# Kernel optimization log

Measured on AMD Instinct MI355X. Metric: run time of the kernel, lower is better.

Reference implementation:

```python
import jax, jax.numpy as jnp
import numpy as np

B, S, D, H = 2, 2048, 1024, 16
DK = D // H  # 64


def setup_inputs() -> dict:
    key = jax.random.key(0)
    ks = jax.random.split(key, 4)
    scale = 1.0 / np.sqrt(D)
    return {
        "q_input": jax.random.normal(ks[0], (B, S, D), dtype=jnp.float32),
        "W_q": jax.random.normal(ks[1], (D, D), dtype=jnp.float32) * scale,
        "b_q": jnp.zeros((D,), dtype=jnp.float32),
        "W_k": jax.random.normal(ks[2], (D, D), dtype=jnp.float32) * scale,
        "b_k": jnp.zeros((D,), dtype=jnp.float32),
        "W_v": jax.random.normal(ks[3], (D, D), dtype=jnp.float32) * scale,
        "b_v": jnp.zeros((D,), dtype=jnp.float32),
    }


def reference(q_input, W_q, b_q, W_k, b_k, W_v, b_v):
    # Self-attention: k_input and v_input default to q_input in the torch module.
    # nn.Linear computes x @ W.T + b
    q = q_input @ W_q.T + b_q
    k = q_input @ W_k.T + b_k
    v = q_input @ W_v.T + b_v

    # [B,S,D] -> [B,H,S,DK]
    def split_heads(x):
        return x.reshape(B, S, H, DK).transpose(0, 2, 1, 3)

    qh, kh, vh = split_heads(q), split_heads(k), split_heads(v)

    # scores [B,H,S,S]; causal mask added BEFORE scaling (as in source; -inf invariant)
    scores = jnp.einsum("bhqd,bhkd->bhqk", qh, kh)
    causal = jnp.tril(jnp.ones((S, S), dtype=bool))
    scores = jnp.where(causal[None, None], scores, -jnp.inf)
    scores = scores / jnp.sqrt(jnp.float32(DK))
    probs = jax.nn.softmax(scores, axis=-1)
    z = jnp.einsum("bhqk,bhkd->bhqd", probs, vh)  # [B,H,S,DK]
    # [B,H,S,DK] -> [B,S,H,DK] -> [B,S,D]
    return z.transpose(0, 2, 1, 3).reshape(B, S, D)
```

## Files before the change

### kernel.cpp

```cpp
#include <hip/hip_runtime.h>
#include <hip/hip_bf16.h>
#include <stdint.h>

typedef __attribute__((ext_vector_type(8))) short short8;
typedef __attribute__((ext_vector_type(4))) short short4v;
typedef __attribute__((ext_vector_type(4))) float f32x4;

#define B_ 2
#define S_ 2048
#define D_ 1024
#define H_ 16
#define DK_ 64
#define M_ (B_*S_)

#define WS_QKV   0
#define WS_XB    12582912
#define WS_WB    16777216

#define QSCALE (0.125f * 1.44269504088896f)

#define GLL16(g, l) __builtin_amdgcn_global_load_lds( \
    (const __attribute__((address_space(1))) void*)(g), \
    (__attribute__((address_space(3))) void*)(l), 16, 0, 0)

#define WAIT_VM0 asm volatile("s_waitcnt vmcnt(0)" ::: "memory")
#define WAIT_VM4 asm volatile("s_waitcnt vmcnt(4)" ::: "memory")
#define WAIT_VM8 asm volatile("s_waitcnt vmcnt(8)" ::: "memory")
#define WAIT_LGKM0 asm volatile("s_waitcnt lgkmcnt(0)" ::: "memory")
#define BARRIER_RAW asm volatile("s_barrier" ::: "memory")

static __device__ __forceinline__ short f2bf(float f){
  union { float f; unsigned u; } x; x.f = f;
  unsigned r = x.u + 0x7fff + ((x.u >> 16) & 1);
  return (short)(r >> 16);
}

__global__ __launch_bounds__(256) void cvt_bf16(
    const float* __restrict__ X,  const float* __restrict__ Wq,
    const float* __restrict__ Wk, const float* __restrict__ Wv,
    short* __restrict__ ws)
{
  const int z = blockIdx.z;
  const float* src; short* dst; int n;
  if (z == 0)      { src = X;  dst = ws + WS_XB;               n = M_*D_; }
  else if (z == 1) { src = Wq; dst = ws + WS_WB;               n = D_*D_; }
  else if (z == 2) { src = Wk; dst = ws + WS_WB + D_*D_;       n = D_*D_; }
  else             { src = Wv; dst = ws + WS_WB + 2*(D_*D_);   n = D_*D_; }
  const int stride = gridDim.x * blockDim.x * 4;
  for (int i = (blockIdx.x * blockDim.x + threadIdx.x) * 4; i < n; i += stride) {
    float4 v = *(const float4*)(src + i);
    short4v o;
    o.x = f2bf(v.x); o.y = f2bf(v.y); o.z = f2bf(v.z); o.w = f2bf(v.w);
    *(short4v*)(dst + i) = o;
  }
}

__global__ __launch_bounds__(512, 2) void qkv_gemm(
    const short* __restrict__ ws_in,
    const float* __restrict__ bq, const float* __restrict__ bk,
    const float* __restrict__ bv, short* __restrict__ qkv)
{
  const int z = blockIdx.z;
  const short* X  = ws_in + WS_XB;
  const short* Wm = ws_in + WS_WB + (size_t)z * (D_*D_);
  short* out = qkv + (size_t)z * (M_*D_);

  __shared__ __align__(16) short lds[65536];

  const int t = threadIdx.x;
  const int w = t >> 6, lane = t & 63;
  const int quad = lane >> 4, l16 = lane & 15;
  const int wm = w >> 2, wn = w & 3;
  const int m0 = blockIdx.y * 256, n0 = blockIdx.x * 256;

  const int rl = t >> 2;
  const int sl = (t & 3) ^ (rl & 3);
  const short* sA0 = X  + (size_t)(m0 + rl) * D_ + sl*8;
  const short* sA1 = sA0 + (size_t)128 * D_;
  const short* sB0 = Wm + (size_t)(n0 + rl) * D_ + sl*8;
  const short* sB1 = sB0 + (size_t)128 * D_;
  const int ldsw = w << 9;

  const int swz = quad ^ (l16 & 3);

  f32x4 acc[8][4];
  #pragma unroll
  for (int i=0;i<8;i++)
    #pragma unroll
    for (int j=0;j<4;j++) acc[i][j] = (f32x4){0.f,0.f,0.f,0.f};

  #pragma unroll
  for (int p=0;p<3;p++){
    GLL16(sA0 + p*32, lds + p*16384 + ldsw);
    GLL16(sA1 + p*32, lds + p*16384 + 4096 + ldsw);
    GLL16(sB0 + p*32, lds + p*16384 + 8192 + ldsw);
    GLL16(sB1 + p*32, lds + p*16384 + 12288 + ldsw);
  }
  WAIT_VM8;
  BARRIER_RAW;

  for (int kt = 0; kt < 32; kt++) {
    const int bf = kt & 3;
    const short* bufA = lds + bf*16384;
    const short* bufB = bufA + 8192;
    const int tb = (kt + 3) & 3;
    const int ko2 = (kt + 3) * 32;
    const bool st = (kt + 3) < 32;

    short8 aF[4], bF[4];
    #pragma unroll
    for (int mf=0; mf<4; mf++)
      aF[mf] = *(const short8*)(bufA + (wm*128 + mf*16 + l16)*32 + swz*8);
    #pragma unroll
    for (int nf=0; nf<4; nf++)
      bF[nf] = *(const short8*)(bufB + (wn*64 + nf*16 + l16)*32 + swz*8);
    if (st) {
      GLL16(sA0 + ko2, lds + tb*16384 + ldsw);
      GLL16(sA1 + ko2, lds + tb*16384 + 4096 + ldsw);
    }
    BARRIER_RAW;
    WAIT_LGKM0;
    __builtin_amdgcn_s_setprio(1);
    #pragma unroll
    for (int mf=0; mf<4; mf++)
      #pragma unroll
      for (int nf=0; nf<4; nf++)
        acc[mf][nf] = __builtin_amdgcn_mfma_f32_16x16x32_bf16(aF[mf], bF[nf], acc[mf][nf], 0,0,0);
    __builtin_amdgcn_s_setprio(0);
    BARRIER_RAW;

    #pragma unroll
    for (int mf=0; mf<4; mf++)
      aF[mf] = *(const short8*)(bufA + (wm*128 + 64 + mf*16 + l16)*32 + swz*8);
    if (st) {
      GLL16(sB0 + ko2, lds + tb*16384 + 8192 + ldsw);
      GLL16(sB1 + ko2, lds + tb*16384 + 12288 + ldsw);
    }
    BARRIER_RAW;
    WAIT_LGKM0;
    __builtin_amdgcn_s_setprio(1);
    #pragma unroll
    for (int mf=0; mf<4; mf++)
      #pragma unroll
      for (int nf=0; nf<4; nf++)
        acc[4+mf][nf] = __builtin_amdgcn_mfma_f32_16x16x32_bf16(aF[mf], bF[nf], acc[4+mf][nf], 0,0,0);
    __builtin_amdgcn_s_setprio(0);
    if      (kt < 29)  { WAIT_VM8; }
    else if (kt == 29) { WAIT_VM4; }
    else if (kt == 30) { WAIT_VM0; }
    BARRIER_RAW;
  }

  __syncthreads();

  if (z != 2) {
    const float scale = (z==0) ? QSCALE : 1.0f;
    const float* bias = (z==0) ? bq : bk;
    float bv4[4];
    #pragma unroll
    for (int nf=0; nf<4; nf++) bv4[nf] = bias[n0 + wn*64 + nf*16 + l16];
    short* ep = lds;
    #pragma unroll
    for (int p=0; p<2; p++){
      if (wm == p){
        #pragma unroll
        for (int mf=0; mf<8; mf++)
          #pragma unroll
          for (int nf=0; nf<4; nf++)
            #pragma unroll
            for (int i=0; i<4; i++)
              ep[(mf*16 + quad*4 + i)*264 + wn*64 + nf*16 + l16] =
                  f2bf((acc[mf][nf][i] + bv4[nf]) * scale);
      }
      __syncthreads();
      #pragma unroll
      for (int it=0; it<8; it++){
        const int cid = it*512 + t;
        const int row = cid >> 5, cc = cid & 31;
        short8 vv = *(const short8*)(ep + row*264 + cc*8);
        const int m = m0 + p*128 + row, bidx = m >> 11, s = m & 2047;
        const int n = n0 + cc*8, h = n >> 6, dd = n & 63;
        *(short8*)(out + (((size_t)(bidx*H_ + h))*S_ + s)*DK_ + dd) = vv;
      }
      __syncthreads();
    }
  } else {
    float bv4[4];
    #pragma unroll
    for (int nf=0; nf<4; nf++) bv4[nf] = bv[n0 + wn*64 + nf*16 + l16];
    short* ep = lds;
    #pragma unroll
    for (int p=0; p<2; p++){
      if (wm == p){
        #pragma unroll
        for (int mf=0; mf<8; mf++)
          #pragma unroll
          for (int nf=0; nf<4; nf++)
            #pragma unroll
            for (int i=0; i<4; i++)
              ep[(wn*64 + nf*16 + l16)*136 + mf*16 + quad*4 + i] =
                  f2bf(acc[mf][nf][i] + bv4[nf]);
      }
      __syncthreads();
      #pragma unroll
      for (int it=0; it<8; it++){
        const int cid = it*512 + t;
        const int row = cid >> 4, cc = cid & 15;
        short8 vv = *(const short8*)(ep + row*136 + cc*8);
        const int n = n0 + row, h = n >> 6, dd = n & 63;
        const int m0p = m0 + p*128;
        const int bidx = m0p >> 11;
        const int s = (m0p & 2047) + cc*8;
        *(short8*)(out + (((size_t)(bidx*H_ + h))*DK_ + dd)*S_ + s) = vv;
      }
      __syncthreads();
    }
  }
}

__global__ __launch_bounds__(256, 3) void attn(
    const short* __restrict__ qkv, float* __restrict__ out)
{
  const int bh = blockIdx.y;
  const int qt = (gridDim.x - 1) - blockIdx.x;
  const short* Q  = qkv + (size_t)bh * (S_*DK_);
  const short* K  = Q + (size_t)(M_*D_);
  const short* VT = qkv + (size_t)(2*M_*D_) + (size_t)bh * (DK_*S_);

  __shared__ short Kbuf[2][4096];
  __shared__ short Vbuf[2][4096];
  __shared__ short Ps[8192];

  const int t = threadIdx.x;
  const int w = t >> 6, lane = t & 63;
  const int quad = lane >> 4, l16 = lane & 15;
  const int sw = l16 & 7;
  const int lr = lane >> 3, lc = lane & 7;
  const int csrc = lc ^ lr;

  short8 bq[2][2];
  #pragma unroll
  for (int kc=0;kc<2;kc++)
    #pragma unroll
    for (int mt=0;mt<2;mt++)
      bq[kc][mt] = *(const short8*)(Q + (size_t)(qt*128 + w*32 + mt*16 + l16)*DK_
                                      + (kc*4 + quad)*8);

  const int nkt = 2*qt + 2;
  #pragma unroll
  for (int j=0;j<2;j++){
    const int rb = (j*4 + w)*8;
    GLL16(K  + (size_t)(rb + lr)*DK_ + csrc*8, &Kbuf[0][0] + rb*64);
    GLL16(VT + (size_t)(rb + lr)*S_  + csrc*8, &Vbuf[0][0] + rb*64);
  }

  f32x4 o[2][4];
  float lsum[2];
  #pragma unroll
  for (int mt=0;mt<2;mt++){
    #pragma unroll
    for (int nd=0;nd<4;nd++) o[mt][nd] = (f32x4){0.f,0.f,0.f,0.f};
    lsum[mt] = 0.f;
  }

  const int pw_half = (quad & 1) * 4;
  const int pw_ckb  = quad >> 1;
  int cur = 0;

  for (int kt = 0; kt < nkt; kt++){
    WAIT_VM0;
    BARRIER_RAW;
    const int nxt = cur ^ 1;
    if (kt + 1 < nkt) {
      const int kb2 = (kt+1)*64;
      short* Kn = &Kbuf[nxt][0];
      short* Vn = &Vbuf[nxt][0];
      #pragma unroll
      for (int j=0;j<2;j++){
        const int rb = (j*4 + w)*8;
        GLL16(K  + (size_t)(kb2 + rb + lr)*DK_ + csrc*8, Kn + rb*64);
        GLL16(VT + (size_t)(rb + lr)*S_ + kb2 + csrc*8,  Vn + rb*64);
      }
    }
    const short* Kc = &Kbuf[cur][0];
    const short* Vc = &Vbuf[cur][0];
    const int kb = kt*64;

    f32x4 sc[4][2];
    #pragma unroll
    for (int ntk=0;ntk<4;ntk++)
      #pragma unroll
      for (int mt=0;mt<2;mt++) sc[ntk][mt] = (f32x4){0.f,0.f,0.f,0.f};
    #pragma unroll
    for (int kc=0;kc<2;kc++){
      const int xch = (kc*4 + quad) ^ sw;
      short8 ak[4];
      #pragma unroll
      for (int ntk=0;ntk<4;ntk++)
        ak[ntk] = *(const short8*)(Kc + (ntk*16 + l16)*64 + xch*8);
      #pragma unroll
      for (int ntk=0;ntk<4;ntk++)
        #pragma unroll
        for (int mt=0;mt<2;mt++)
          sc[ntk][mt] = __builtin_amdgcn_mfma_f32_16x16x32_bf16(ak[ntk], bq[kc][mt], sc[ntk][mt], 0,0,0);
    }

    const int q0w = qt*128 + w*32;
    if (kb + 63 > q0w) {
      #pragma unroll
      for (int ntk=0;ntk<4;ntk++)
        #pragma unroll
        for (int mt=0;mt<2;mt++){
          const int qg = q0w + mt*16 + l16;
          #pragma unroll
          for (int i=0;i<4;i++){
            const int kg = kb + ntk*16 + quad*4 + i;
            if (kg > qg) sc[ntk][mt][i] = -3.0e38f;
          }
        }
    }

    #pragma unroll
    for (int mt=0;mt<2;mt++){
      const int r = w*32 + mt*16 + l16;
      #pragma unroll
      for (int ntk=0;ntk<4;ntk++){
        float p0 = __builtin_amdgcn_exp2f(sc[ntk][mt][0]);
        float p1 = __builtin_amdgcn_exp2f(sc[ntk][mt][1]);
        float p2 = __builtin_amdgcn_exp2f(sc[ntk][mt][2]);
        float p3 = __builtin_amdgcn_exp2f(sc[ntk][mt][3]);
        lsum[mt] += (p0+p1) + (p2+p3);
        unsigned lo = __builtin_amdgcn_perm(__float_as_uint(p1), __float_as_uint(p0), 0x07060302u);
        unsigned hi = __builtin_amdgcn_perm(__float_as_uint(p3), __float_as_uint(p2), 0x07060302u);
        const int slot = (ntk*2 + pw_ckb) ^ sw;
        *(uint2*)(Ps + r*64 + slot*8 + pw_half) = make_uint2(lo, hi);
      }
    }
    asm volatile("" ::: "memory");

    #pragma unroll
    for (int kc=0;kc<2;kc++){
      const int xch = (kc*4 + quad) ^ sw;
      short8 pa[2], vb[4];
      #pragma unroll
      for (int mt=0;mt<2;mt++)
        pa[mt] = *(const short8*)(Ps + (w*32 + mt*16 + l16)*64 + xch*8);
      #pragma unroll
      for (int nd=0;nd<4;nd++)
        vb[nd] = *(const short8*)(Vc + (nd*16 + l16)*64 + xch*8);
      #pragma unroll
      for (int mt=0;mt<2;mt++)
        #pragma unroll
        for (int nd=0;nd<4;nd++)
          o[mt][nd] = __builtin_amdgcn_mfma_f32_16x16x32_bf16(pa[mt], vb[nd], o[mt][nd], 0,0,0);
    }
    cur = nxt;
  }

  const int bb = bh >> 4, h = bh & 15;
  float linv[2];
  #pragma unroll
  for (int mt=0;mt<2;mt++){
    float rs = lsum[mt];
    rs += __shfl_xor(rs, 16, 64);
    rs += __shfl_xor(rs, 32, 64);
    linv[mt] = 1.0f / rs;
  }
  #pragma unroll
  for (int mt=0;mt<2;mt++){
    #pragma unroll
    for (int i=0;i<4;i++){
      const float lw = __shfl(linv[mt], (quad<<4) + (quad<<2) + i, 64);
      const int q = qt*128 + w*32 + mt*16 + quad*4 + i;
      #pragma unroll
      for (int nd=0;nd<4;nd++){
        const int d = nd*16 + l16;
        out[ ((size_t)bb*S_ + q)*D_ + h*DK_ + d ] = o[mt][nd][i] * lw;
      }
    }
  }
}

extern "C" void kernel_launch(void* const* d_in, const int* in_sizes, int n_in,
                              void* d_out, int out_size, void* d_ws, size_t ws_size,
                              hipStream_t stream)
{
  (void)in_sizes; (void)n_in; (void)out_size; (void)ws_size;
  const float* X  = (const float*)d_in[0];
  const float* Wq = (const float*)d_in[1];
  const float* bq = (const float*)d_in[2];
  const float* Wk = (const float*)d_in[3];
  const float* bk = (const float*)d_in[4];
  const float* Wv = (const float*)d_in[5];
  const float* bv = (const float*)d_in[6];
  short* ws  = (short*)d_ws;
  float* out = (float*)d_out;

  dim3 g0(1024, 1, 4);
  cvt_bf16<<<g0, dim3(256,1,1), 0, stream>>>(X, Wq, Wk, Wv, ws);
  dim3 g1(D_/256, M_/256, 3);
  qkv_gemm<<<g1, dim3(512,1,1), 0, stream>>>(ws, bq, bk, bv, ws + WS_QKV);
  dim3 g2(S_/128, B_*H_);
  attn<<<g2, dim3(256,1,1), 0, stream>>>(ws + WS_QKV, out);
}
```

Baseline: 176.4 us.

## Rewrite attention with 32x32 MFMA, register-resident P, and 256-row query tiles

Switches the attention kernel from 16x16x32 to 32x32x16 bf16 MFMA tiles and grows each block to 512 threads covering 256 query rows. The probabilities now go straight from the score accumulators into the PV A-operand through v_cvt_pk_bf16 and v_permlane32_swap, which removes the LDS round-trip and its shared buffer. Warps whose key tile lies wholly above the causal diagonal skip their compute but still take part in the loads and barriers. The cost is fewer blocks, which means less parallelism and coarser causal load balance across the grid, plus more work per warp.

```diff
diff --git a/kernel.cpp b/kernel.cpp
--- a/kernel.cpp
+++ b/kernel.cpp
@@ -5,6 +5,7 @@
 typedef __attribute__((ext_vector_type(8))) short short8;
 typedef __attribute__((ext_vector_type(4))) short short4v;
 typedef __attribute__((ext_vector_type(4))) float f32x4;
+typedef __attribute__((ext_vector_type(16))) float f32x16;
 
 #define B_ 2
 #define S_ 2048
@@ -218,166 +219,126 @@
   }
 }
 
-__global__ __launch_bounds__(256, 3) void attn(
+__global__ __launch_bounds__(512, 2) void attn(
     const short* __restrict__ qkv, float* __restrict__ out)
 {
   const int bh = blockIdx.y;
-  const int qt = (gridDim.x - 1) - blockIdx.x;
+  const int qt = 7 - blockIdx.x;
   const short* Q  = qkv + (size_t)bh * (S_*DK_);
   const short* K  = Q + (size_t)(M_*D_);
   const short* VT = qkv + (size_t)(2*M_*D_) + (size_t)bh * (DK_*S_);
 
   __shared__ short Kbuf[2][4096];
   __shared__ short Vbuf[2][4096];
-  __shared__ short Ps[8192];
 
   const int t = threadIdx.x;
   const int w = t >> 6, lane = t & 63;
-  const int quad = lane >> 4, l16 = lane & 15;
-  const int sw = l16 & 7;
-  const int lr = lane >> 3, lc = lane & 7;
-  const int csrc = lc ^ lr;
-
-  short8 bq[2][2];
+  const int l32 = lane & 31, h = lane >> 5;
+
+  const int q0w = qt*256 + w*32;
+
+  short8 bq[4];
   #pragma unroll
-  for (int kc=0;kc<2;kc++)
-    #pragma unroll
-    for (int mt=0;mt<2;mt++)
-      bq[kc][mt] = *(const short8*)(Q + (size_t)(qt*128 + w*32 + mt*16 + l16)*DK_
-                                      + (kc*4 + quad)*8);
-
-  const int nkt = 2*qt + 2;
-  #pragma unroll
-  for (int j=0;j<2;j++){
-    const int rb = (j*4 + w)*8;
-    GLL16(K  + (size_t)(rb + lr)*DK_ + csrc*8, &Kbuf[0][0] + rb*64);
-    GLL16(VT + (size_t)(rb + lr)*S_  + csrc*8, &Vbuf[0][0] + rb*64);
-  }
-
-  f32x4 o[2][4];
-  float lsum[2];
-  #pragma unroll
-  for (int mt=0;mt<2;mt++){
-    #pragma unroll
-    for (int nd=0;nd<4;nd++) o[mt][nd] = (f32x4){0.f,0.f,0.f,0.f};
-    lsum[mt] = 0.f;
-  }
-
-  const int pw_half = (quad & 1) * 4;
-  const int pw_ckb  = quad >> 1;
-  int cur = 0;
+  for (int dc=0; dc<4; dc++)
+    bq[dc] = *(const short8*)(Q + (size_t)(q0w + l32)*DK_ + dc*16 + h*8);
+
+  const int sr  = w*8 + (lane >> 3);
+  const int sc8 = ((lane & 7) ^ (lane >> 3)) * 8;
+
+  const int nkt = 4*(qt+1);
+  GLL16(K  + (size_t)sr*DK_ + sc8, &Kbuf[0][0] + w*512);
+  GLL16(VT + (size_t)sr*S_  + sc8, &Vbuf[0][0] + w*512);
+
+  f32x16 o0 = {0.f,0.f,0.f,0.f,0.f,0.f,0.f,0.f,0.f,0.f,0.f,0.f,0.f,0.f,0.f,0.f};
+  f32x16 o1 = o0;
+  float lsum = 0.f;
+  const int xrow = l32 & 7;
 
   for (int kt = 0; kt < nkt; kt++){
+    const int cur = kt & 1;
     WAIT_VM0;
     BARRIER_RAW;
-    const int nxt = cur ^ 1;
     if (kt + 1 < nkt) {
       const int kb2 = (kt+1)*64;
-      short* Kn = &Kbuf[nxt][0];
-      short* Vn = &Vbuf[nxt][0];
-      #pragma unroll
-      for (int j=0;j<2;j++){
-        const int rb = (j*4 + w)*8;
-        GLL16(K  + (size_t)(kb2 + rb + lr)*DK_ + csrc*8, Kn + rb*64);
-        GLL16(VT + (size_t)(rb + lr)*S_ + kb2 + csrc*8,  Vn + rb*64);
-      }
-    }
+      GLL16(K  + (size_t)(kb2 + sr)*DK_ + sc8, &Kbuf[cur^1][0] + w*512);
+      GLL16(VT + (size_t)sr*S_ + kb2 + sc8,    &Vbuf[cur^1][0] + w*512);
+    }
+    const int kb = kt*64;
+    if (kb > q0w + 31) continue;
+
     const short* Kc = &Kbuf[cur][0];
     const short* Vc = &Vbuf[cur][0];
-    const int kb = kt*64;
-
-    f32x4 sc[4][2];
-    #pragma unroll
-    for (int ntk=0;ntk<4;ntk++)
-      #pragma unroll
-      for (int mt=0;mt<2;mt++) sc[ntk][mt] = (f32x4){0.f,0.f,0.f,0.f};
-    #pragma unroll
-    for (int kc=0;kc<2;kc++){
-      const int xch = (kc*4 + quad) ^ sw;
-      short8 ak[4];
-      #pragma unroll
-      for (int ntk=0;ntk<4;ntk++)
-        ak[ntk] = *(const short8*)(Kc + (ntk*16 + l16)*64 + xch*8);
-      #pragma unroll
-      for (int ntk=0;ntk<4;ntk++)
-        #pragma unroll
-        for (int mt=0;mt<2;mt++)
-          sc[ntk][mt] = __builtin_amdgcn_mfma_f32_16x16x32_bf16(ak[ntk], bq[kc][mt], sc[ntk][mt], 0,0,0);
-    }
-
-    const int q0w = qt*128 + w*32;
+
+    f32x16 s[2];
+    s[0] = o0 - o0;
+    s[1] = s[0];
+    #pragma unroll
+    for (int dc=0; dc<4; dc++){
+      const int xk = ((dc*2 + h) ^ xrow)*8;
+      short8 a0 = *(const short8*)(Kc + l32*64 + xk);
+      short8 a1 = *(const short8*)(Kc + (32 + l32)*64 + xk);
+      s[0] = __builtin_amdgcn_mfma_f32_32x32x16_bf16(a0, bq[dc], s[0], 0,0,0);
+      s[1] = __builtin_amdgcn_mfma_f32_32x32x16_bf16(a1, bq[dc], s[1], 0,0,0);
+    }
+
     if (kb + 63 > q0w) {
-      #pragma unroll
-      for (int ntk=0;ntk<4;ntk++)
-        #pragma unroll
-        for (int mt=0;mt<2;mt++){
-          const int qg = q0w + mt*16 + l16;
-          #pragma unroll
-          for (int i=0;i<4;i++){
-            const int kg = kb + ntk*16 + quad*4 + i;
-            if (kg > qg) sc[ntk][mt][i] = -3.0e38f;
-          }
-        }
-    }
-
-    #pragma unroll
-    for (int mt=0;mt<2;mt++){
-      const int r = w*32 + mt*16 + l16;
-      #pragma unroll
-      for (int ntk=0;ntk<4;ntk++){
-        float p0 = __builtin_amdgcn_exp2f(sc[ntk][mt][0]);
-        float p1 = __builtin_amdgcn_exp2f(sc[ntk][mt][1]);
-        float p2 = __builtin_amdgcn_exp2f(sc[ntk][mt][2]);
-        float p3 = __builtin_amdgcn_exp2f(sc[ntk][mt][3]);
-        lsum[mt] += (p0+p1) + (p2+p3);
-        unsigned lo = __builtin_amdgcn_perm(__float_as_uint(p1), __float_as_uint(p0), 0x07060302u);
-        unsigned hi = __builtin_amdgcn_perm(__float_as_uint(p3), __float_as_uint(p2), 0x07060302u);
-        const int slot = (ntk*2 + pw_ckb) ^ sw;
-        *(uint2*)(Ps + r*64 + slot*8 + pw_half) = make_uint2(lo, hi);
-      }
-    }
-    asm volatile("" ::: "memory");
-
-    #pragma unroll
-    for (int kc=0;kc<2;kc++){
-      const int xch = (kc*4 + quad) ^ sw;
-      short8 pa[2], vb[4];
-      #pragma unroll
-      for (int mt=0;mt<2;mt++)
-        pa[mt] = *(const short8*)(Ps + (w*32 + mt*16 + l16)*64 + xch*8);
-      #pragma unroll
-      for (int nd=0;nd<4;nd++)
-        vb[nd] = *(const short8*)(Vc + (nd*16 + l16)*64 + xch*8);
-      #pragma unroll
-      for (int mt=0;mt<2;mt++)
-        #pragma unroll
-        for (int nd=0;nd<4;nd++)
-          o[mt][nd] = __builtin_amdgcn_mfma_f32_16x16x32_bf16(pa[mt], vb[nd], o[mt][nd], 0,0,0);
-    }
-    cur = nxt;
-  }
-
-  const int bb = bh >> 4, h = bh & 15;
-  float linv[2];
+      const int qg = q0w + l32;
+      #pragma unroll
+      for (int r=0; r<16; r++){
+        const int k0 = kb + (r&3) + 8*(r>>2) + 4*h;
+        if (k0      > qg) s[0][r] = -3.0e38f;
+        if (k0 + 32 > qg) s[1][r] = -3.0e38f;
+      }
+    }
+
+    short8 pf[4];
+    #pragma unroll
+    for (int mk=0; mk<2; mk++){
+      #pragma unroll
+      for (int u=0; u<2; u++){
+        float p0 = __builtin_amdgcn_exp2f(s[mk][8*u+0]);
+        float p1 = __builtin_amdgcn_exp2f(s[mk][8*u+1]);
+        float p2 = __builtin_amdgcn_exp2f(s[mk][8*u+2]);
+        float p3 = __builtin_amdgcn_exp2f(s[mk][8*u+3]);
+        float p4 = __builtin_amdgcn_exp2f(s[mk][8*u+4]);
+        float p5 = __builtin_amdgcn_exp2f(s[mk][8*u+5]);
+        float p6 = __builtin_amdgcn_exp2f(s[mk][8*u+6]);
+        float p7 = __builtin_amdgcn_exp2f(s[mk][8*u+7]);
+        lsum += ((p0+p1)+(p2+p3)) + ((p4+p5)+(p6+p7));
+        unsigned X0, X1, Y0, Y1;
+        asm("v_cvt_pk_bf16_f32 %0, %1, %2" : "=v"(X0) : "v"(p0), "v"(p1));
+        asm("v_cvt_pk_bf16_f32 %0, %1, %2" : "=v"(X1) : "v"(p2), "v"(p3));
+        asm("v_cvt_pk_bf16_f32 %0, %1, %2" : "=v"(Y0) : "v"(p4), "v"(p5));
+        asm("v_cvt_pk_bf16_f32 %0, %1, %2" : "=v"(Y1) : "v"(p6), "v"(p7));
+        asm("v_permlane32_swap_b32 %0, %1" : "+v"(X0), "+v"(Y0));
+        asm("v_permlane32_swap_b32 %0, %1" : "+v"(X1), "+v"(Y1));
+        union { unsigned u4[4]; short8 s8; } pp;
+        pp.u4[0] = X0; pp.u4[1] = X1; pp.u4[2] = Y0; pp.u4[3] = Y1;
+        pf[mk*2 + u] = pp.s8;
+      }
+    }
+
+    #pragma unroll
+    for (int kk=0; kk<4; kk++){
+      const int xv = ((kk*2 + h) ^ xrow)*8;
+      short8 v0 = *(const short8*)(Vc + l32*64 + xv);
+      short8 v1 = *(const short8*)(Vc + (32 + l32)*64 + xv);
+      o0 = __builtin_amdgcn_mfma_f32_32x32x16_bf16(pf[kk], v0, o0, 0,0,0);
+      o1 = __builtin_amdgcn_mfma_f32_32x32x16_bf16(pf[kk], v1, o1, 0,0,0);
+    }
+  }
+
+  float rs = lsum + __shfl_xor(lsum, 32, 64);
+  float linv = 1.0f / rs;
+  const int bb = bh >> 4, hh = bh & 15;
   #pragma unroll
-  for (int mt=0;mt<2;mt++){
-    float rs = lsum[mt];
-    rs += __shfl_xor(rs, 16, 64);
-    rs += __shfl_xor(rs, 32, 64);
-    linv[mt] = 1.0f / rs;
-  }
-  #pragma unroll
-  for (int mt=0;mt<2;mt++){
-    #pragma unroll
-    for (int i=0;i<4;i++){
-      const float lw = __shfl(linv[mt], (quad<<4) + (quad<<2) + i, 64);
-      const int q = qt*128 + w*32 + mt*16 + quad*4 + i;
-      #pragma unroll
-      for (int nd=0;nd<4;nd++){
-        const int d = nd*16 + l16;
-        out[ ((size_t)bb*S_ + q)*D_ + h*DK_ + d ] = o[mt][nd][i] * lw;
-      }
-    }
+  for (int r=0; r<16; r++){
+    const int qrow = (r&3) + 8*(r>>2) + 4*h;
+    const float lw = __shfl(linv, qrow, 64);
+    const int qg = q0w + qrow;
+    float* dst = out + ((size_t)bb*S_ + qg)*D_ + hh*DK_;
+    dst[l32]      = o0[r] * lw;
+    dst[32 + l32] = o1[r] * lw;
   }
 }
 
@@ -400,6 +361,6 @@
   cvt_bf16<<<g0, dim3(256,1,1), 0, stream>>>(X, Wq, Wk, Wv, ws);
   dim3 g1(D_/256, M_/256, 3);
   qkv_gemm<<<g1, dim3(512,1,1), 0, stream>>>(ws, bq, bk, bv, ws + WS_QKV);
-  dim3 g2(S_/128, B_*H_);
-  attn<<<g2, dim3(256,1,1), 0, stream>>>(ws + WS_QKV, out);
-}
+  dim3 g2(8, B_*H_);
+  attn<<<g2, dim3(512,1,1), 0, stream>>>(ws + WS_QKV, out);
+}
```

Measured after the change: 175.2 us. No clear change (-0.7%).
